# Performance work log

Measured on AMD Instinct MI355X. Metric: run time of the kernel, lower is better.

The kernel has to match this reference:

```python
import jax, jax.numpy as jnp
import numpy as np
from jax import lax

NFEATS = 128
NMODES = 2
KH = KW = 3


def _conv_lstm_step(h, c, inp, W, b):
    """Standard ConvLSTMCell: conv over [inp, h] -> 4 gates -> c/h update.
    inp: (B, Cin, H, W); h, c: (B, nfeats, H, W); W: (4*nfeats, Cin+nfeats, 3, 3)."""
    z = lax.conv_general_dilated(
        jnp.concatenate([inp, h], axis=1), W,
        window_strides=(1, 1), padding='SAME',
        dimension_numbers=('NCHW', 'OIHW', 'NCHW'))
    z = z + b[None, :, None, None]
    i, f, o, g = jnp.split(z, 4, axis=1)
    c_next = jax.nn.sigmoid(f) * c + jax.nn.sigmoid(i) * jnp.tanh(g)
    h_next = jax.nn.sigmoid(o) * jnp.tanh(c_next)
    return h_next, c_next


def setup_inputs() -> dict:
    key = jax.random.key(0)
    ks = jax.random.split(key, 8)
    B, T, H, Wsp = 4, 8, 32, 32
    x1 = jax.random.normal(ks[0], (B, T, NFEATS, H, Wsp), dtype=jnp.float32)
    x2 = jax.random.normal(ks[1], (B, T, NFEATS, H, Wsp), dtype=jnp.float32)
    s = 0.02
    W1 = jax.random.normal(ks[2], (4 * NFEATS, NMODES * NFEATS + NFEATS, KH, KW), dtype=jnp.float32) * s
    b1 = jnp.zeros((4 * NFEATS,), dtype=jnp.float32)
    W2 = jax.random.normal(ks[3], (4 * NFEATS, 2 * NFEATS, KH, KW), dtype=jnp.float32) * s
    b2 = jnp.zeros((4 * NFEATS,), dtype=jnp.float32)
    W3 = jax.random.normal(ks[4], (4 * NFEATS, 2 * NFEATS, KH, KW), dtype=jnp.float32) * s
    b3 = jnp.zeros((4 * NFEATS,), dtype=jnp.float32)
    return {"x1": x1, "x2": x2, "W1": W1, "b1": b1, "W2": W2, "b2": b2, "W3": W3, "b3": b3}


def reference(x1, x2, W1, b1, W2, b2, W3, b3):
    # cat modalities on channel dim: (B, T, nmodes*nfeats, H, W)
    x = jnp.concatenate([x1, x2], axis=2)
    B, T, C, H, Wsp = x.shape
    zero = jnp.zeros((B, NFEATS, H, Wsp), dtype=x.dtype)
    carry0 = (zero, zero, zero, zero, zero, zero)  # h1,c1,h2,c2,h3,c3
    xs = jnp.moveaxis(x, 1, 0)  # (T, B, C, H, W)

    def step(carry, xt):
        h1, c1, h2, c2, h3, c3 = carry
        h1, c1 = _conv_lstm_step(h1, c1, xt, W1, b1)
        h2, c2 = _conv_lstm_step(h2, c2, h1, W2, b2)
        h3, c3 = _conv_lstm_step(h3, c3, h2, W3, b3)
        return (h1, c1, h2, c2, h3, c3), None

    (h1, c1, h2, c2, h3, c3), _ = lax.scan(step, carry0, xs)
    return h3
```

## Files before the change

### kernel.cpp

```cpp
#include <hip/hip_runtime.h>
#include <hip/hip_bf16.h>

typedef unsigned short u16;
typedef __attribute__((ext_vector_type(8))) short short8;
typedef __attribute__((ext_vector_type(4))) float floatx4;

__device__ __forceinline__ u16 f2bf(float x) {
  unsigned u = __float_as_uint(x);
  u += 0x7fffu + ((u >> 16) & 1u);
  return (u16)(u >> 16);
}
__device__ __forceinline__ float bf2f(u16 u) {
  return __uint_as_float(((unsigned)u) << 16);
}
__device__ __forceinline__ float sigm(float x) {
  return 1.0f / (1.0f + __expf(-x));
}


__global__ __launch_bounds__(256) void xsplit_kernel(
    const float* __restrict__ x1, const float* __restrict__ x2,
    u16* __restrict__ Xh, u16* __restrict__ Xl)
{
  __shared__ float lds[128][65];
  int bx  = blockIdx.x;
  int sel = bx >> 9;
  int rem = bx & 511;
  int bt  = rem >> 4;
  int pg  = rem & 15;
  int b = bt >> 3, t = bt & 7;
  int p0 = pg << 6;
  const float* src = (sel ? x2 : x1) + ((size_t)bt << 17);
  int tid = threadIdx.x;
  #pragma unroll
  for (int k2 = 0; k2 < 8; ++k2) {
    int idx = tid + (k2 << 8);
    int c = idx >> 4, p4 = (idx & 15) << 2;
    floatx4 v = *reinterpret_cast<const floatx4*>(src + ((size_t)c << 10) + p0 + p4);
    lds[c][p4] = v[0]; lds[c][p4 + 1] = v[1]; lds[c][p4 + 2] = v[2]; lds[c][p4 + 3] = v[3];
  }
  __syncthreads();
  int pl = tid >> 2;
  int cg = (tid & 3) << 5;
  size_t obase = (((size_t)((t * 4 + b) * 1024 + p0 + pl)) << 8) + (sel << 7) + cg;
  #pragma unroll
  for (int q = 0; q < 4; ++q) {
    short8 hv, lv;
    #pragma unroll
    for (int j = 0; j < 8; ++j) {
      float f = lds[cg + q * 8 + j][pl];
      u16 h = f2bf(f);
      hv[j] = (short)h;
      lv[j] = (short)f2bf(f - bf2f(h));
    }
    *reinterpret_cast<short8*>(Xh + obase + q * 8) = hv;
    *reinterpret_cast<short8*>(Xl + obase + q * 8) = lv;
  }
}

__global__ __launch_bounds__(256) void wsplit_kernel(
    const float* __restrict__ W, u16* __restrict__ Wh, u16* __restrict__ Wl, int CIN)
{
  int K = CIN * 9;
  int i = blockIdx.x * 256 + threadIdx.x;
  int np = i / K;
  int k = i - np * K;
  int e9 = k / CIN;
  int ci = k - e9 * CIN;
  int n = (np & 3) * 128 + (np >> 2);
  float v = W[((size_t)n * CIN + ci) * 9 + e9];
  size_t o = ((size_t)((np >> 4) * (K >> 3) + (k >> 3)) * 16 + (np & 15)) * 8 + (k & 7);
  u16 h = f2bf(v);
  Wh[o] = h;
  Wl[o] = f2bf(v - bf2f(h));
}

__global__ __launch_bounds__(256) void init_state(
    float* __restrict__ c1, float* __restrict__ c2, float* __restrict__ c3,
    u16* __restrict__ h1h, u16* __restrict__ h1l,
    u16* __restrict__ h2h, u16* __restrict__ h2l,
    u16* __restrict__ h3h, u16* __restrict__ h3l)
{
  int i = blockIdx.x * 256 + threadIdx.x;
  c1[i] = 0.f; c2[i] = 0.f; c3[i] = 0.f;
  h1h[i] = 0; h1l[i] = 0; h2h[i] = 0; h2l[i] = 0; h3h[i] = 0; h3l[i] = 0;
}

template<bool FUSE>
__global__ __launch_bounds__(256, 2) void conv_gemm(
    const u16* __restrict__ A1h, const u16* __restrict__ A1l, int CA,
    const u16* __restrict__ A2h, const u16* __restrict__ A2l, int CB,
    const u16* __restrict__ Wh, const u16* __restrict__ Wl,
    int WCIN, int wcoff, int WK,
    float* __restrict__ zout,
    const float* __restrict__ zx,
    const float* __restrict__ bias,
    float* __restrict__ c, u16* __restrict__ hh, u16* __restrict__ hl,
    float* __restrict__ hout)
{
  const int CIN = CA + CB;
  __shared__ __align__(16) char smem[34816];

  int tid = threadIdx.x;
  int bx  = blockIdx.x;
  int nt = bx & 3;
  int mt = bx >> 2;
  int m0 = mt * 64;
  int slot = m0 >> 10;
  int pbase = m0 & 1023;
  int y0 = pbase >> 5;
  int n0 = nt * 128;

  int lane = tid & 63, wid = tid >> 6;
  int nh = wid & 1, kh = wid >> 1;
  int fr = lane & 15, kq = lane >> 4;
  const int WK8 = WK >> 3;
  const int g16b = (n0 >> 4) + nh * 4;

  floatx4 acc[4][4];
  #pragma unroll
  for (int i2 = 0; i2 < 4; ++i2)
    #pragma unroll
    for (int j2 = 0; j2 < 4; ++j2)
      acc[i2][j2] = (floatx4)0.0f;

  short8 RH[5], RL[5];
  const int NC = CIN >> 6;

  auto ldA = [&](int cc) {
    const u16 *sh, *sl; int cbase, CH;
    if (cc < CA) { sh = A1h; sl = A1l; cbase = cc;      CH = CA; }
    else         { sh = A2h; sl = A2l; cbase = cc - CA; CH = CB; }
    #pragma unroll
    for (int r = 0; r < 5; ++r) {
      int u = tid + 256 * r;
      if (u < 1088) {
        int prow = u >> 3, cq = u & 7;
        int hrow = prow / 34;
        int xcol = prow - hrow * 34;
        int y = y0 - 1 + hrow;
        int x = xcol - 1;
        bool valid = ((unsigned)y < 32u) & ((unsigned)x < 32u);
        short8 vh = (short8)0, vl = (short8)0;
        if (valid) {
          size_t ab = (size_t)(slot * 1024 + y * 32 + x) * CH + cbase + cq * 8;
          vh = *reinterpret_cast<const short8*>(sh + ab);
          vl = *reinterpret_cast<const short8*>(sl + ab);
        }
        RH[r] = vh; RL[r] = vl;
      }
    }
  };

  auto stA = [&]() {
    #pragma unroll
    for (int r = 0; r < 5; ++r) {
      int u = tid + 256 * r;
      if (u < 1088) {
        int prow = u >> 3, cq = u & 7;
        int off = prow * 128 + (((cq ^ (prow & 7)) & 7) << 4);
        *reinterpret_cast<short8*>(smem + off)         = RH[r];
        *reinterpret_cast<short8*>(smem + 17408 + off) = RL[r];
      }
    }
  };

  auto computeChunk = [&](int cc) {
    const int u0 = kh ? 9 : 0;
    short8 Bch[4], Bcl[4];
    {
      int e9 = u0 >> 1, ks = u0 & 1;
      int kb = wcoff + e9 * WCIN + cc + ks * 32 + kq * 8;
      #pragma unroll
      for (int nf = 0; nf < 4; ++nf) {
        size_t bo = ((size_t)((g16b + nf) * WK8 + (kb >> 3)) * 16 + fr) * 8;
        Bch[nf] = *reinterpret_cast<const short8*>(Wh + bo);
        Bcl[nf] = *reinterpret_cast<const short8*>(Wl + bo);
      }
    }
    #pragma unroll 1
    for (int ui = 0; ui < 9; ++ui) {
      int u = u0 + ui;
      int e9 = u >> 1, ks = u & 1;
      short8 Bnh_[4], Bnl_[4];
      if (ui < 8) {
        int un = u + 1;
        int kb = wcoff + (un >> 1) * WCIN + cc + (un & 1) * 32 + kq * 8;
        #pragma unroll
        for (int nf = 0; nf < 4; ++nf) {
          size_t bo = ((size_t)((g16b + nf) * WK8 + (kb >> 3)) * 16 + fr) * 8;
          Bnh_[nf] = *reinterpret_cast<const short8*>(Wh + bo);
          Bnl_[nf] = *reinterpret_cast<const short8*>(Wl + bo);
        }
      }
      int dy = e9 / 3 - 1;
      int dx = e9 - (e9 / 3) * 3 - 1;
      short8 Ah_[4], Al_[4];
      #pragma unroll
      for (int mf = 0; mf < 4; ++mf) {
        int ar = mf * 16 + fr;
        int prow = ((ar >> 5) + 1 + dy) * 34 + (ar & 31) + 1 + dx;
        int off = prow * 128 + ((((ks * 4 + kq) ^ (prow & 7)) & 7) << 4);
        Ah_[mf] = *reinterpret_cast<const short8*>(smem + off);
        Al_[mf] = *reinterpret_cast<const short8*>(smem + 17408 + off);
      }
      __builtin_amdgcn_s_setprio(1);
      #pragma unroll
      for (int mf = 0; mf < 4; ++mf)
        #pragma unroll
        for (int nf = 0; nf < 4; ++nf)
          acc[mf][nf] = __builtin_amdgcn_mfma_f32_16x16x32_bf16(Ah_[mf], Bch[nf], acc[mf][nf], 0, 0, 0);
      #pragma unroll
      for (int mf = 0; mf < 4; ++mf)
        #pragma unroll
        for (int nf = 0; nf < 4; ++nf)
          acc[mf][nf] = __builtin_amdgcn_mfma_f32_16x16x32_bf16(Ah_[mf], Bcl[nf], acc[mf][nf], 0, 0, 0);
      #pragma unroll
      for (int mf = 0; mf < 4; ++mf)
        #pragma unroll
        for (int nf = 0; nf < 4; ++nf)
          acc[mf][nf] = __builtin_amdgcn_mfma_f32_16x16x32_bf16(Al_[mf], Bch[nf], acc[mf][nf], 0, 0, 0);
      __builtin_amdgcn_s_setprio(0);
      if (ui < 8) {
        #pragma unroll
        for (int nf = 0; nf < 4; ++nf) { Bch[nf] = Bnh_[nf]; Bcl[nf] = Bnl_[nf]; }
      }
    }
  };

  ldA(0); stA();
  for (int q = 0; q < NC; ++q) {
    if (q + 1 < NC) ldA((q + 1) << 6);
    __syncthreads();
    computeChunk(q << 6);
    __syncthreads();
    if (q + 1 < NC) stA();
  }

  float (*tr)[68] = reinterpret_cast<float(*)[68]>(smem + nh * 17408);
  if (kh == 0) {
    #pragma unroll
    for (int mf = 0; mf < 4; ++mf)
      #pragma unroll
      for (int nf = 0; nf < 4; ++nf)
        #pragma unroll
        for (int r = 0; r < 4; ++r)
          tr[mf * 16 + kq * 4 + r][nf * 16 + fr] = acc[mf][nf][r];
  }
  __syncthreads();
  if (kh == 1) {
    #pragma unroll
    for (int mf = 0; mf < 4; ++mf)
      #pragma unroll
      for (int nf = 0; nf < 4; ++nf)
        #pragma unroll
        for (int r = 0; r < 4; ++r)
          tr[mf * 16 + kq * 4 + r][nf * 16 + fr] += acc[mf][nf][r];
  }
  __syncthreads();

  int m = lane;
  int ppix = pbase + m;
  size_t grow = (size_t)slot * 1024 + ppix;

  if (!FUSE) {
    size_t zrow = ((size_t)(m0 + m) << 9) + n0 + nh * 64 + kh * 32;
    #pragma unroll
    for (int j = 0; j < 8; ++j) {
      floatx4 v = *reinterpret_cast<const floatx4*>(&tr[m][kh * 32 + j * 4]);
      *reinterpret_cast<floatx4*>(zout + zrow + j * 4) = v;
    }
    return;
  }

  short8 hhv, hlv;
  floatx4 cv4[2];
  #pragma unroll
  for (int j = 0; j < 8; ++j) {
    int oc = kh * 8 + j;
    int ocg = nt * 32 + nh * 16 + oc;
    float zg[4];
    floatx4 tv = *reinterpret_cast<const floatx4*>(&tr[m][oc * 4]);
    if (zx) {
      floatx4 zv = *reinterpret_cast<const floatx4*>(zx + (grow << 9) + n0 + nh * 64 + oc * 4);
      #pragma unroll
      for (int g = 0; g < 4; ++g) zg[g] = tv[g] + zv[g] + bias[g * 128 + ocg];
    } else {
      #pragma unroll
      for (int g = 0; g < 4; ++g) zg[g] = tv[g] + bias[g * 128 + ocg];
    }
    size_t cidx = grow * 128 + ocg;
    float cvl = c[cidx];
    float cn = sigm(zg[1]) * cvl + sigm(zg[0]) * tanhf(zg[3]);
    float hn = sigm(zg[2]) * tanhf(cn);
    cv4[j >> 2][j & 3] = cn;
    u16 hb = f2bf(hn);
    hhv[j] = (short)hb;
    hlv[j] = (short)f2bf(hn - bf2f(hb));
    if (hout) hout[((size_t)slot * 128 + ocg) * 1024 + ppix] = hn;
  }
  size_t obase = grow * 128 + nt * 32 + nh * 16 + kh * 8;
  *reinterpret_cast<floatx4*>(c + obase)     = cv4[0];
  *reinterpret_cast<floatx4*>(c + obase + 4) = cv4[1];
  *reinterpret_cast<short8*>(hh + obase) = hhv;
  *reinterpret_cast<short8*>(hl + obase) = hlv;
}

extern "C" void kernel_launch(void* const* d_in, const int* in_sizes, int n_in,
                              void* d_out, int out_size, void* d_ws, size_t ws_size,
                              hipStream_t stream)
{
  const float* x1 = (const float*)d_in[0];
  const float* x2 = (const float*)d_in[1];
  const float* W1 = (const float*)d_in[2];
  const float* b1 = (const float*)d_in[3];
  const float* W2 = (const float*)d_in[4];
  const float* b2 = (const float*)d_in[5];
  const float* W3 = (const float*)d_in[6];
  const float* b3 = (const float*)d_in[7];
  float* out = (float*)d_out;

  char* ws = (char*)d_ws;
  size_t off = 0;
  auto alloc = [&](size_t bytes) {
    char* p = ws + off;
    off += (bytes + 255) & ~(size_t)255;
    return p;
  };
  u16*   Xh  = (u16*)  alloc(16777216);
  u16*   Xl  = (u16*)  alloc(16777216);
  u16*   W1h = (u16*)  alloc(3538944);
  u16*   W1l = (u16*)  alloc(3538944);
  u16*   W2h = (u16*)  alloc(2359296);
  u16*   W2l = (u16*)  alloc(2359296);
  u16*   W3h = (u16*)  alloc(2359296);
  u16*   W3l = (u16*)  alloc(2359296);
  u16*   hb_[12];
  for (int i = 0; i < 12; ++i) hb_[i] = (u16*)alloc(1048576);
  float* c1  = (float*)alloc(2097152);
  float* c2  = (float*)alloc(2097152);
  float* c3  = (float*)alloc(2097152);
  float* zx  = (float*)alloc(67108864);
  if (off > ws_size) return;

  u16 **h1h = &hb_[0], **h1l = &hb_[2], **h2h = &hb_[4], **h2l = &hb_[6],
      **h3h = &hb_[8], **h3l = &hb_[10];

  xsplit_kernel<<<1024, 256, 0, stream>>>(x1, x2, Xh, Xl);
  wsplit_kernel<<<6912, 256, 0, stream>>>(W1, W1h, W1l, 384);
  wsplit_kernel<<<4608, 256, 0, stream>>>(W2, W2h, W2l, 256);
  wsplit_kernel<<<4608, 256, 0, stream>>>(W3, W3h, W3l, 256);
  init_state<<<2048, 256, 0, stream>>>(c1, c2, c3,
      hb_[0], hb_[2], hb_[4], hb_[6], hb_[8], hb_[10]);

  conv_gemm<false><<<2048, 256, 0, stream>>>(
      Xh, Xl, 256, nullptr, nullptr, 0, W1h, W1l, 384, 0, 3456,
      zx, nullptr, nullptr, nullptr, nullptr, nullptr, nullptr);

  for (int t = 0; t < 8; ++t) {
    int pi = t & 1, po = pi ^ 1;
    const float* zxt = zx + (size_t)t * 2097152;
    conv_gemm<true><<<256, 256, 0, stream>>>(
        h1h[pi], h1l[pi], 128, nullptr, nullptr, 0, W1h, W1l, 384, 256, 3456,
        nullptr, zxt, b1, c1, h1h[po], h1l[po], nullptr);
    conv_gemm<true><<<256, 256, 0, stream>>>(
        h1h[po], h1l[po], 128, h2h[pi], h2l[pi], 128, W2h, W2l, 256, 0, 2304,
        nullptr, nullptr, b2, c2, h2h[po], h2l[po], nullptr);
    conv_gemm<true><<<256, 256, 0, stream>>>(
        h2h[po], h2l[po], 128, h3h[pi], h3l[pi], 128, W3h, W3l, 256, 0, 2304,
        nullptr, nullptr, b3, c3, h3h[po], h3l[po], (t == 7) ? out : nullptr);
  }
}
```

Before: 1.159 ms.

## Template conv GEMM on row-tile height to double recurrent-step grid size

```diff
diff --git a/kernel.cpp b/kernel.cpp
--- a/kernel.cpp
+++ b/kernel.cpp
@@ -3,6 +3,7 @@
 
 typedef unsigned short u16;
 typedef __attribute__((ext_vector_type(8))) short short8;
+typedef __attribute__((ext_vector_type(4))) short short4v;
 typedef __attribute__((ext_vector_type(4))) float floatx4;
 
 __device__ __forceinline__ u16 f2bf(float x) {
@@ -86,26 +87,31 @@
   h1h[i] = 0; h1l[i] = 0; h2h[i] = 0; h2l[i] = 0; h3h[i] = 0; h3l[i] = 0;
 }
 
-template<bool FUSE>
-__global__ __launch_bounds__(256, 2) void conv_gemm(
+template<bool FUSE, int YR, int BPC>
+__global__ __launch_bounds__(256, BPC) void conv_gemm(
     const u16* __restrict__ A1h, const u16* __restrict__ A1l, int CA,
     const u16* __restrict__ A2h, const u16* __restrict__ A2l, int CB,
     const u16* __restrict__ Wh, const u16* __restrict__ Wl,
-    int WCIN, int wcoff, int WK,
+    int WCIN, int wcoff, int WK, int MT,
     float* __restrict__ zout,
     const float* __restrict__ zx,
     const float* __restrict__ bias,
     float* __restrict__ c, u16* __restrict__ hh, u16* __restrict__ hl,
     float* __restrict__ hout)
 {
+  constexpr int PROWS = (YR + 2) * 34;
+  constexpr int HALOB = PROWS * 128;
+  constexpr int MF = 2 * YR;
+  constexpr int RLD = (PROWS * 8 + 255) / 256;
   const int CIN = CA + CB;
-  __shared__ __align__(16) char smem[34816];
+
+  __shared__ __align__(16) char smem[2 * HALOB];
 
   int tid = threadIdx.x;
   int bx  = blockIdx.x;
-  int nt = bx & 3;
-  int mt = bx >> 2;
-  int m0 = mt * 64;
+  int nt = bx / MT;
+  int mt = bx - nt * MT;
+  int m0 = mt * (32 * YR);
   int slot = m0 >> 10;
   int pbase = m0 & 1023;
   int y0 = pbase >> 5;
@@ -117,14 +123,14 @@
   const int WK8 = WK >> 3;
   const int g16b = (n0 >> 4) + nh * 4;
 
-  floatx4 acc[4][4];
+  floatx4 acc[MF][4];
   #pragma unroll
-  for (int i2 = 0; i2 < 4; ++i2)
+  for (int i2 = 0; i2 < MF; ++i2)
     #pragma unroll
     for (int j2 = 0; j2 < 4; ++j2)
       acc[i2][j2] = (floatx4)0.0f;
 
-  short8 RH[5], RL[5];
+  short8 RH[RLD], RL[RLD];
   const int NC = CIN >> 6;
 
   auto ldA = [&](int cc) {
@@ -132,9 +138,9 @@
     if (cc < CA) { sh = A1h; sl = A1l; cbase = cc;      CH = CA; }
     else         { sh = A2h; sl = A2l; cbase = cc - CA; CH = CB; }
     #pragma unroll
-    for (int r = 0; r < 5; ++r) {
+    for (int r = 0; r < RLD; ++r) {
       int u = tid + 256 * r;
-      if (u < 1088) {
+      if (u < PROWS * 8) {
         int prow = u >> 3, cq = u & 7;
         int hrow = prow / 34;
         int xcol = prow - hrow * 34;
@@ -154,13 +160,13 @@
 
   auto stA = [&]() {
     #pragma unroll
-    for (int r = 0; r < 5; ++r) {
+    for (int r = 0; r < RLD; ++r) {
       int u = tid + 256 * r;
-      if (u < 1088) {
+      if (u < PROWS * 8) {
         int prow = u >> 3, cq = u & 7;
         int off = prow * 128 + (((cq ^ (prow & 7)) & 7) << 4);
         *reinterpret_cast<short8*>(smem + off)         = RH[r];
-        *reinterpret_cast<short8*>(smem + 17408 + off) = RL[r];
+        *reinterpret_cast<short8*>(smem + HALOB + off) = RL[r];
       }
     }
   };
@@ -169,8 +175,7 @@
     const int u0 = kh ? 9 : 0;
     short8 Bch[4], Bcl[4];
     {
-      int e9 = u0 >> 1, ks = u0 & 1;
-      int kb = wcoff + e9 * WCIN + cc + ks * 32 + kq * 8;
+      int kb = wcoff + (u0 >> 1) * WCIN + cc + (u0 & 1) * 32 + kq * 8;
       #pragma unroll
       for (int nf = 0; nf < 4; ++nf) {
         size_t bo = ((size_t)((g16b + nf) * WK8 + (kb >> 3)) * 16 + fr) * 8;
@@ -195,28 +200,28 @@
       }
       int dy = e9 / 3 - 1;
       int dx = e9 - (e9 / 3) * 3 - 1;
-      short8 Ah_[4], Al_[4];
-      #pragma unroll
-      for (int mf = 0; mf < 4; ++mf) {
+      short8 Ah_[MF], Al_[MF];
+      #pragma unroll
+      for (int mf = 0; mf < MF; ++mf) {
         int ar = mf * 16 + fr;
         int prow = ((ar >> 5) + 1 + dy) * 34 + (ar & 31) + 1 + dx;
         int off = prow * 128 + ((((ks * 4 + kq) ^ (prow & 7)) & 7) << 4);
         Ah_[mf] = *reinterpret_cast<const short8*>(smem + off);
-        Al_[mf] = *reinterpret_cast<const short8*>(smem + 17408 + off);
+        Al_[mf] = *reinterpret_cast<const short8*>(smem + HALOB + off);
       }
       __builtin_amdgcn_s_setprio(1);
       #pragma unroll
-      for (int mf = 0; mf < 4; ++mf)
+      for (int mf = 0; mf < MF; ++mf)
         #pragma unroll
         for (int nf = 0; nf < 4; ++nf)
           acc[mf][nf] = __builtin_amdgcn_mfma_f32_16x16x32_bf16(Ah_[mf], Bch[nf], acc[mf][nf], 0, 0, 0);
       #pragma unroll
-      for (int mf = 0; mf < 4; ++mf)
+      for (int mf = 0; mf < MF; ++mf)
         #pragma unroll
         for (int nf = 0; nf < 4; ++nf)
           acc[mf][nf] = __builtin_amdgcn_mfma_f32_16x16x32_bf16(Ah_[mf], Bcl[nf], acc[mf][nf], 0, 0, 0);
       #pragma unroll
-      for (int mf = 0; mf < 4; ++mf)
+      for (int mf = 0; mf < MF; ++mf)
         #pragma unroll
         for (int nf = 0; nf < 4; ++nf)
           acc[mf][nf] = __builtin_amdgcn_mfma_f32_16x16x32_bf16(Al_[mf], Bch[nf], acc[mf][nf], 0, 0, 0);
@@ -237,10 +242,10 @@
     if (q + 1 < NC) stA();
   }
 
-  float (*tr)[68] = reinterpret_cast<float(*)[68]>(smem + nh * 17408);
+  float (*tr)[68] = reinterpret_cast<float(*)[68]>(smem + nh * HALOB);
   if (kh == 0) {
     #pragma unroll
-    for (int mf = 0; mf < 4; ++mf)
+    for (int mf = 0; mf < MF; ++mf)
       #pragma unroll
       for (int nf = 0; nf < 4; ++nf)
         #pragma unroll
@@ -250,7 +255,7 @@
   __syncthreads();
   if (kh == 1) {
     #pragma unroll
-    for (int mf = 0; mf < 4; ++mf)
+    for (int mf = 0; mf < MF; ++mf)
       #pragma unroll
       for (int nf = 0; nf < 4; ++nf)
         #pragma unroll
@@ -259,25 +264,28 @@
   }
   __syncthreads();
 
-  int m = lane;
+  int m  = (YR == 1) ? (lane & 31) : lane;
+  int ol = (YR == 1) ? (lane >> 5) : 0;
   int ppix = pbase + m;
   size_t grow = (size_t)slot * 1024 + ppix;
 
   if (!FUSE) {
-    size_t zrow = ((size_t)(m0 + m) << 9) + n0 + nh * 64 + kh * 32;
-    #pragma unroll
-    for (int j = 0; j < 8; ++j) {
-      floatx4 v = *reinterpret_cast<const floatx4*>(&tr[m][kh * 32 + j * 4]);
+    size_t zrow = ((size_t)(m0 + m) << 9) + n0 + nh * 64 + kh * 32 + ol * 16;
+    constexpr int NJ = (YR == 1) ? 4 : 8;
+    #pragma unroll
+    for (int j = 0; j < NJ; ++j) {
+      floatx4 v = *reinterpret_cast<const floatx4*>(&tr[m][kh * 32 + ol * 16 + j * 4]);
       *reinterpret_cast<floatx4*>(zout + zrow + j * 4) = v;
     }
     return;
   }
 
-  short8 hhv, hlv;
-  floatx4 cv4[2];
+  constexpr int NJ = (YR == 1) ? 4 : 8;
+  int obc = kh * 8 + ol * 4;
+  float cnv[NJ], hnv[NJ];
   #pragma unroll
-  for (int j = 0; j < 8; ++j) {
-    int oc = kh * 8 + j;
+  for (int j = 0; j < NJ; ++j) {
+    int oc = obc + j;
     int ocg = nt * 32 + nh * 16 + oc;
     float zg[4];
     floatx4 tv = *reinterpret_cast<const floatx4*>(&tr[m][oc * 4]);
@@ -293,17 +301,36 @@
     float cvl = c[cidx];
     float cn = sigm(zg[1]) * cvl + sigm(zg[0]) * tanhf(zg[3]);
     float hn = sigm(zg[2]) * tanhf(cn);
-    cv4[j >> 2][j & 3] = cn;
-    u16 hb = f2bf(hn);
-    hhv[j] = (short)hb;
-    hlv[j] = (short)f2bf(hn - bf2f(hb));
+    cnv[j] = cn; hnv[j] = hn;
     if (hout) hout[((size_t)slot * 128 + ocg) * 1024 + ppix] = hn;
   }
-  size_t obase = grow * 128 + nt * 32 + nh * 16 + kh * 8;
-  *reinterpret_cast<floatx4*>(c + obase)     = cv4[0];
-  *reinterpret_cast<floatx4*>(c + obase + 4) = cv4[1];
-  *reinterpret_cast<short8*>(hh + obase) = hhv;
-  *reinterpret_cast<short8*>(hl + obase) = hlv;
+  size_t obase = grow * 128 + nt * 32 + nh * 16 + obc;
+  if constexpr (YR == 1) {
+    floatx4 cv; short4v hv, lv;
+    #pragma unroll
+    for (int j = 0; j < 4; ++j) {
+      cv[j] = cnv[j];
+      u16 hb = f2bf(hnv[j]);
+      hv[j] = (short)hb;
+      lv[j] = (short)f2bf(hnv[j] - bf2f(hb));
+    }
+    *reinterpret_cast<floatx4*>(c + obase) = cv;
+    *reinterpret_cast<short4v*>(hh + obase) = hv;
+    *reinterpret_cast<short4v*>(hl + obase) = lv;
+  } else {
+    floatx4 cv[2]; short8 hv, lv;
+    #pragma unroll
+    for (int j = 0; j < 8; ++j) {
+      cv[j >> 2][j & 3] = cnv[j];
+      u16 hb = f2bf(hnv[j]);
+      hv[j] = (short)hb;
+      lv[j] = (short)f2bf(hnv[j] - bf2f(hb));
+    }
+    *reinterpret_cast<floatx4*>(c + obase)     = cv[0];
+    *reinterpret_cast<floatx4*>(c + obase + 4) = cv[1];
+    *reinterpret_cast<short8*>(hh + obase) = hv;
+    *reinterpret_cast<short8*>(hl + obase) = lv;
+  }
 }
 
 extern "C" void kernel_launch(void* const* d_in, const int* in_sizes, int n_in,
@@ -353,21 +380,21 @@
   init_state<<<2048, 256, 0, stream>>>(c1, c2, c3,
       hb_[0], hb_[2], hb_[4], hb_[6], hb_[8], hb_[10]);
 
-  conv_gemm<false><<<2048, 256, 0, stream>>>(
-      Xh, Xl, 256, nullptr, nullptr, 0, W1h, W1l, 384, 0, 3456,
+  conv_gemm<false, 2, 3><<<2048, 256, 0, stream>>>(
+      Xh, Xl, 256, nullptr, nullptr, 0, W1h, W1l, 384, 0, 3456, 512,
       zx, nullptr, nullptr, nullptr, nullptr, nullptr, nullptr);
 
   for (int t = 0; t < 8; ++t) {
     int pi = t & 1, po = pi ^ 1;
     const float* zxt = zx + (size_t)t * 2097152;
-    conv_gemm<true><<<256, 256, 0, stream>>>(
-        h1h[pi], h1l[pi], 128, nullptr, nullptr, 0, W1h, W1l, 384, 256, 3456,
+    conv_gemm<true, 1, 2><<<512, 256, 0, stream>>>(
+        h1h[pi], h1l[pi], 128, nullptr, nullptr, 0, W1h, W1l, 384, 256, 3456, 128,
         nullptr, zxt, b1, c1, h1h[po], h1l[po], nullptr);
-    conv_gemm<true><<<256, 256, 0, stream>>>(
-        h1h[po], h1l[po], 128, h2h[pi], h2l[pi], 128, W2h, W2l, 256, 0, 2304,
+    conv_gemm<true, 1, 2><<<512, 256, 0, stream>>>(
+        h1h[po], h1l[po], 128, h2h[pi], h2l[pi], 128, W2h, W2l, 256, 0, 2304, 128,
         nullptr, nullptr, b2, c2, h2h[po], h2l[po], nullptr);
-    conv_gemm<true><<<256, 256, 0, stream>>>(
-        h2h[po], h2l[po], 128, h3h[pi], h3l[pi], 128, W3h, W3l, 256, 0, 2304,
+    conv_gemm<true, 1, 2><<<512, 256, 0, stream>>>(
+        h2h[po], h2l[po], 128, h3h[pi], h3l[pi], 128, W3h, W3l, 256, 0, 2304, 128,
         nullptr, nullptr, b3, c3, h3h[po], h3l[po], (t == 7) ? out : nullptr);
   }
 }
```

New measurement: 1.205 ms. +4.0%, slower.
